# Optimization experiments

Measured on AMD Instinct MI355X. Metric: run time of the kernel, lower is better.

## Reference

```python
import jax, jax.numpy as jnp
import numpy as np

NUM_HEADS, KEY_DIM, BLOCK, HALO = 8, 64, 8, 4
KV_KERNEL = BLOCK + 2 * HALO  # 16
EMB = NUM_HEADS * KEY_DIM     # 512


def setup_inputs() -> dict:
    key = jax.random.key(0)
    k = jax.random.split(key, 6)
    stddev = KEY_DIM ** -0.5
    return {
        "x": jax.random.normal(k[0], (8, 64, 64, 512), jnp.float32),
        "wq": jax.random.normal(k[1], (512, EMB), jnp.float32) * 0.02,
        "wkv": jax.random.normal(k[2], (512, 2 * EMB), jnp.float32) * 0.02,
        "wout": jax.random.normal(k[3], (EMB, EMB), jnp.float32) * 0.02,
        "pos_w": jax.random.normal(k[4], (KEY_DIM, 2 * KV_KERNEL - 1), jnp.float32) * stddev,
        "pos_h": jax.random.normal(k[5], (KEY_DIM, 2 * KV_KERNEL - 1), jnp.float32) * stddev,
    }


def rel_to_abs(rel):
    # rel: [B, N, hh, ww, 2*pos_dim-1] -> [B, N, hh, ww, pos_dim]
    b, n, hh, ww, dim = rel.shape
    pos_dim = (dim + 1) // 2
    gap = pos_dim - ww
    flat = rel.reshape(b, n, hh, ww * dim)[:, :, :, ww - 1:-1]
    return flat.reshape(b, n, hh, ww, 2 * (pos_dim - 1))[:, :, :, :, gap:pos_dim + gap]


def halo_forward(x, wq, wkv, wout, pos_w, pos_h):
    B, H, W, C = x.shape
    h, w = H // BLOCK, W // BLOCK
    K = KV_KERNEL
    scale = 1.0 / jnp.sqrt(jnp.asarray(KEY_DIM, x.dtype))

    # Query: [B, hd, h, w, block^2, key_dim]
    q = (x @ wq) * scale
    q = q.reshape(B, h, BLOCK, w, BLOCK, NUM_HEADS, KEY_DIM)
    attn_q = q.transpose(0, 5, 1, 3, 2, 4, 6).reshape(B, NUM_HEADS, h, w, BLOCK * BLOCK, KEY_DIM)

    # Overlapping halo KV windows (im2col-style gather, like tf.image.extract_patches)
    kv = x @ wkv
    kv_p = jnp.pad(kv, ((0, 0), (HALO, HALO), (HALO, HALO), (0, 0)))
    idx_h = jnp.arange(h)[:, None] * BLOCK + jnp.arange(K)[None, :]  # [h, K]
    idx_w = jnp.arange(w)[:, None] * BLOCK + jnp.arange(K)[None, :]  # [w, K]
    patches = kv_p[:, idx_h][:, :, :, idx_w]          # [B, h, K, w, K, 2*EMB]
    patches = patches.transpose(0, 1, 3, 2, 4, 5)     # [B, h, w, K, K, 2*EMB]
    patches = patches.reshape(B, h, w, K * K, NUM_HEADS, 2 * KEY_DIM)
    patches = patches.transpose(0, 4, 1, 2, 3, 5)     # [B, hd, h, w, K^2, 2*key_dim]
    key_t, val = patches[..., :KEY_DIM], patches[..., KEY_DIM:]

    scores = jnp.einsum('bnhwqc,bnhwkc->bnhwqk', attn_q, key_t)  # [B,hd,h,w,bq,bk]

    # Relative position logits (width + height), query already carries qk_scale
    pos_q = attn_q.reshape(B, NUM_HEADS * h * w, BLOCK, BLOCK, KEY_DIM)
    rel_w = rel_to_abs(pos_q @ pos_w)                                      # [B,N,hb,wb,K]
    rel_h = rel_to_abs(pos_q.transpose(0, 1, 3, 2, 4) @ pos_h)
    rel_h = rel_h.transpose(0, 1, 3, 2, 4)                                 # [B,N,hb,wb,K]
    pos = rel_w[..., None, :] + rel_h[..., :, None]                        # [B,N,hb,wb,Kh,Kw]
    pos = pos.reshape(B, NUM_HEADS, h, w, BLOCK * BLOCK, K * K)

    attn = jax.nn.softmax(scores + pos, axis=-1)
    out = jnp.einsum('bnhwqk,bnhwkc->bnhwqc', attn, val)
    out = out.reshape(B, NUM_HEADS, h, w, BLOCK, BLOCK, KEY_DIM)
    out = out.transpose(0, 2, 4, 3, 5, 1, 6).reshape(B, H, W, EMB)
    return out @ wout


def reference(x, wq, wkv, wout, pos_w, pos_h):
    return halo_forward(x, wq, wkv, wout, pos_w, pos_h)
```

## Files before the change

kernel.cpp:

```cpp
#include <hip/hip_runtime.h>
#include <hip/hip_fp16.h>
#include <math.h>

typedef _Float16 f16x8 __attribute__((ext_vector_type(8)));
typedef _Float16 f16x4 __attribute__((ext_vector_type(4)));
typedef float    f32x4 __attribute__((ext_vector_type(4)));

#define M_TOT 32768
#define VROW  4608

__device__ __forceinline__ void gload16(const void* g, void* l) {
    __builtin_amdgcn_global_load_lds(
        (const __attribute__((address_space(1))) unsigned int*)g,
        (__attribute__((address_space(3))) unsigned int*)l, 16, 0, 0);
}

__device__ __forceinline__ f32x4 mfma32(f16x8 a, f16x8 b, f32x4 c) {
    return __builtin_amdgcn_mfma_f32_16x16x32_f16(a, b, c, 0, 0, 0);
}

__global__ __launch_bounds__(256) void conv_x(const float* __restrict__ x,
                                              __half* __restrict__ y) {
    const size_t i = ((size_t)blockIdx.x * 256 + threadIdx.x) * 8;
    float4 a = *(const float4*)&x[i];
    float4 b = *(const float4*)&x[i + 4];
    __half2 h[4];
    h[0] = __floats2half2_rn(a.x, a.y);
    h[1] = __floats2half2_rn(a.z, a.w);
    h[2] = __floats2half2_rn(b.x, b.y);
    h[3] = __floats2half2_rn(b.z, b.w);
    *(float4*)&y[i] = *(float4*)h;
}

__global__ __launch_bounds__(256) void conv_w(const float* __restrict__ wq,
                                              const float* __restrict__ wkv,
                                              const float* __restrict__ wout,
                                              __half* __restrict__ wT,
                                              __half* __restrict__ woT) {
    const int id = blockIdx.x * 256 + threadIdx.x;
    const int nr = id >> 9, k = id & 511;
    if (nr < 512) {
        wT[(size_t)nr * 512 + k]  = __float2half(wq[k * 512 + nr] * 0.125f);
    } else if (nr < 1536) {
        wT[(size_t)nr * 512 + k]  = __float2half(wkv[k * 1024 + (nr - 512)]);
    } else {
        woT[(size_t)(nr - 1536) * 512 + k] = __float2half(wout[k * 512 + (nr - 1536)]);
    }
}

__global__ __launch_bounds__(256) void pos_prep(const float* __restrict__ posw,
                                                const float* __restrict__ posh,
                                                __half* __restrict__ posT) {
    const int id = blockIdx.x * 256 + threadIdx.x;
    const int tb = id >> 11, idx = (id >> 6) & 31, d = id & 63;
    const float* src = tb ? posh : posw;
    posT[id] = __float2half((idx < 31) ? src[d * 31 + idx] : 0.f);
}

__global__ __launch_bounds__(256) void vborder(__half* __restrict__ vTp) {
    const int id = blockIdx.x * 256 + threadIdx.x;
    const int row = id >> 7, rem = id & 127;
    const int y = rem >> 1, side = rem & 1;
    f16x4 z = {(_Float16)0.f, (_Float16)0.f, (_Float16)0.f, (_Float16)0.f};
    *(f16x4*)(vTp + (size_t)row * VROW + y * 72 + side * 68) = z;
}

template <int MODE, int NBN>
__global__ __launch_bounds__(256) void mfma_gemm(
    const __half* __restrict__ A, const __half* __restrict__ Bt,
    __half* __restrict__ q16, __half* __restrict__ k16, __half* __restrict__ vTp,
    float* __restrict__ outf)
{
    __shared__ __align__(16) char As[128 * 128];
    __shared__ __align__(16) char Bs[128 * 128];

    const int t = threadIdx.x;
    const int l = t & 63, w = t >> 6;
    const int wr = w >> 1, wc = w & 1;
    const int lr = l & 15, hi = l >> 4;

    const int bid = blockIdx.x;
    const int xcd = bid & 7, loc = bid >> 3;
    const int bm  = xcd * 32 + (loc & 31);
    const int bn  = loc >> 5;

    f32x4 acc[4][4];
    #pragma unroll
    for (int i = 0; i < 4; ++i)
        #pragma unroll
        for (int j = 0; j < 4; ++j) acc[i][j] = (f32x4){0.f, 0.f, 0.f, 0.f};

    const int scid_row[4] = { (t * 16) >> 7, (256 * 16 + t * 16) >> 7,
                              (512 * 16 + t * 16) >> 7, (768 * 16 + t * 16) >> 7 };
    const int sch = (t & 7);

    for (int k0 = 0; k0 < 512; k0 += 64) {
        #pragma unroll
        for (int it = 0; it < 4; ++it) {
            const int row = it * 32 + (t >> 3);
            const int kk  = k0 + ((sch ^ (row & 7)) * 8);
            gload16(A + (size_t)(bm * 128 + row) * 512 + kk,
                    As + (it * 256 + w * 64) * 16);
        }
        #pragma unroll
        for (int it = 0; it < 4; ++it) {
            const int row = it * 32 + (t >> 3);
            const int kk  = k0 + ((sch ^ (row & 7)) * 8);
            gload16(Bt + (size_t)(bn * 128 + row) * 512 + kk,
                    Bs + (it * 256 + w * 64) * 16);
        }
        __syncthreads();

        #pragma unroll
        for (int dc = 0; dc < 2; ++dc) {
            f16x8 af[4], bf[4];
            #pragma unroll
            for (int i = 0; i < 4; ++i) {
                const int ra = wr * 64 + i * 16 + lr;
                af[i] = *(const f16x8*)(As + ra * 128 + (((dc * 4 + hi) ^ (ra & 7)) * 16));
            }
            #pragma unroll
            for (int j = 0; j < 4; ++j) {
                const int rb = wc * 64 + j * 16 + lr;
                bf[j] = *(const f16x8*)(Bs + rb * 128 + (((dc * 4 + hi) ^ (rb & 7)) * 16));
            }
            #pragma unroll
            for (int i = 0; i < 4; ++i)
                #pragma unroll
                for (int j = 0; j < 4; ++j)
                    acc[i][j] = mfma32(af[i], bf[j], acc[i][j]);
        }
        __syncthreads();
    }

    const int lq = hi;
    #pragma unroll
    for (int i = 0; i < 4; ++i) {
        #pragma unroll
        for (int j = 0; j < 4; ++j) {
            const int row0 = bm * 128 + wr * 64 + i * 16 + lq * 4;
            const int col  = bn * 128 + wc * 64 + j * 16 + lr;
            if (MODE == 1) {
                #pragma unroll
                for (int r = 0; r < 4; ++r)
                    outf[(size_t)(row0 + r) * 512 + col] = acc[i][j][r];
            } else if (bn < 4) {
                #pragma unroll
                for (int r = 0; r < 4; ++r)
                    q16[(size_t)(row0 + r) * 512 + col] = __float2half(acc[i][j][r]);
            } else if (wc == 0) {
                const int head = bn - 4, d2 = j * 16 + lr;
                #pragma unroll
                for (int r = 0; r < 4; ++r)
                    k16[(size_t)(row0 + r) * 512 + head * 64 + d2] = __float2half(acc[i][j][r]);
            } else {
                const int head = bn - 4, d2 = j * 16 + lr;
                const int bb = row0 >> 12, pix = row0 & 4095;
                const int py = pix >> 6, px = pix & 63;
                f16x4 pv;
                #pragma unroll
                for (int r = 0; r < 4; ++r) pv[r] = (_Float16)acc[i][j][r];
                *(f16x4*)(vTp + ((size_t)((bb * 8 + head) * 64 + d2)) * VROW + py * 72 + px + 4) = pv;
            }
        }
    }
}

__global__ __launch_bounds__(256, 3) void halo_attn(
    const __half* __restrict__ qbuf, const __half* __restrict__ kbuf,
    const __half* __restrict__ vTp, const __half* __restrict__ posT,
    const __half* __restrict__ zp, __half* __restrict__ obuf)
{
    __shared__ __align__(16) char KP[64 * 520];
    __shared__ float RWT[32][68];
    __shared__ float RHT[32][68];
    __shared__ float red[4][64];
    __shared__ float red2[4][64];

    const int hw = blockIdx.x;
    const int wg = (hw & 7) * 512 + (hw >> 3);
    const int wb = wg & 7, hb = (wg >> 3) & 7, n = (wg >> 6) & 7, b = wg >> 9;
    const int t = threadIdx.x;
    const int l = t & 63, g = t >> 6;
    const int hi = l >> 4, c15 = l & 15;

    #pragma unroll
    for (int it = 0; it < 8; ++it) {
        const int cid = it * 256 + t;
        const int S = cid * 16;
        const int row = S >> 7;
        const int d0h = (((S & 127) >> 4) ^ (row & 7)) * 8;
        const int ky = hb * 8 - 4 + (row >> 4);
        const int kx = wb * 8 - 4 + (row & 15);
        const bool ok = ((unsigned)ky < 64u) && ((unsigned)kx < 64u);
        const __half* src = ok ? (kbuf + ((size_t)((b * 64 + ky) * 64 + kx)) * 512 + n * 64 + d0h)
                               : zp;
        gload16(src, KP + (it * 256 + g * 64) * 16);
    }

    f16x8 vfrag[8];
    {
        const __half* vrow = vTp + ((size_t)((b * 8 + n) * 64 + g * 16 + c15)) * VROW;
        const int xoff = wb * 8 + (hi & 1) * 8;
        #pragma unroll
        for (int kc = 0; kc < 8; ++kc) {
            const int ki = kc * 2 + (hi >> 1);
            const int y = hb * 8 - 4 + ki;
            const __half* p = ((unsigned)y < 64u) ? (vrow + y * 72 + xoff) : zp;
            vfrag[kc] = *(const f16x8*)p;
        }
    }

    f16x8 qreg[4][2];
    #pragma unroll
    for (int qf = 0; qf < 4; ++qf) {
        const int q = qf * 16 + c15;
        const size_t pix = (size_t)((b * 64 + hb * 8 + (q >> 3)) * 64 + wb * 8 + (q & 7));
        #pragma unroll
        for (int dc = 0; dc < 2; ++dc)
            qreg[qf][dc] = *(const f16x8*)(qbuf + pix * 512 + n * 64 + dc * 32 + hi * 8);
    }

    {
        const int tb = g >> 1, ih = g & 1;
        f32x4 accp[4];
        #pragma unroll
        for (int qf = 0; qf < 4; ++qf) accp[qf] = (f32x4){0.f, 0.f, 0.f, 0.f};
        #pragma unroll
        for (int dc = 0; dc < 2; ++dc) {
            const f16x8 a = *(const f16x8*)(posT + tb * 2048 + (ih * 16 + c15) * 64 + dc * 32 + hi * 8);
            #pragma unroll
            for (int qf = 0; qf < 4; ++qf)
                accp[qf] = mfma32(a, qreg[qf][dc], accp[qf]);
        }
        float (*dst)[68] = tb ? RHT : RWT;
        #pragma unroll
        for (int qf = 0; qf < 4; ++qf)
            #pragma unroll
            for (int r = 0; r < 4; ++r)
                dst[ih * 16 + hi * 4 + r][qf * 16 + c15] = accp[qf][r];
    }
    __syncthreads();

    f32x4 accs[4][4];
    #pragma unroll
    for (int kf = 0; kf < 4; ++kf)
        #pragma unroll
        for (int qf = 0; qf < 4; ++qf) accs[kf][qf] = (f32x4){0.f, 0.f, 0.f, 0.f};

    __builtin_amdgcn_s_setprio(1);
    #pragma unroll
    for (int kf = 0; kf < 4; ++kf) {
        const int row = g * 64 + kf * 16 + c15;
        #pragma unroll
        for (int dc = 0; dc < 2; ++dc) {
            const int off = (row * 128 + dc * 64 + hi * 16) ^ ((row & 7) << 4);
            f16x8 a = *(const f16x8*)(KP + off);
            #pragma unroll
            for (int qf = 0; qf < 4; ++qf)
                accs[kf][qf] = mfma32(a, qreg[qf][dc], accs[kf][qf]);
        }
    }
    __builtin_amdgcn_s_setprio(0);

    float mq[4];
    #pragma unroll
    for (int qf = 0; qf < 4; ++qf) {
        const int q = qf * 16 + c15;
        const int qj = q & 7, qi = q >> 3;
        float pa[4], pb[4];
        #pragma unroll
        for (int r = 0; r < 4; ++r)  pa[r] = RWT[hi * 4 + r - qj + 15][q];
        #pragma unroll
        for (int kf = 0; kf < 4; ++kf) pb[kf] = RHT[g * 4 + kf - qi + 15][q];
        float mm = -1e30f;
        #pragma unroll
        for (int kf = 0; kf < 4; ++kf)
            #pragma unroll
            for (int r = 0; r < 4; ++r) {
                const float s = accs[kf][qf][r] + pa[r] + pb[kf];
                accs[kf][qf][r] = s;
                mm = fmaxf(mm, s);
            }
        mm = fmaxf(mm, __shfl_xor(mm, 16));
        mm = fmaxf(mm, __shfl_xor(mm, 32));
        mq[qf] = mm;
    }
    if (l < 16) {
        #pragma unroll
        for (int qf = 0; qf < 4; ++qf) red[g][qf * 16 + l] = mq[qf];
    }
    __syncthreads();

    float sums[4];
    #pragma unroll
    for (int qf = 0; qf < 4; ++qf) {
        const int q = qf * 16 + c15;
        const float mfull = fmaxf(fmaxf(red[0][q], red[1][q]), fmaxf(red[2][q], red[3][q]));
        float ss = 0.f;
        #pragma unroll
        for (int kf = 0; kf < 4; ++kf)
            #pragma unroll
            for (int r = 0; r < 4; ++r) {
                const float p = __expf(accs[kf][qf][r] - mfull);
                accs[kf][qf][r] = p;
                ss += p;
            }
        ss += __shfl_xor(ss, 16);
        ss += __shfl_xor(ss, 32);
        sums[qf] = ss;
        #pragma unroll
        for (int kf = 0; kf < 4; ++kf) {
            __half2 h01 = __floats2half2_rn(accs[kf][qf][0], accs[kf][qf][1]);
            __half2 h23 = __floats2half2_rn(accs[kf][qf][2], accs[kf][qf][3]);
            uint2 wv;
            wv.x = *(unsigned*)&h01;
            wv.y = *(unsigned*)&h23;
            *(uint2*)(KP + q * 520 + (g * 64 + kf * 16 + hi * 4) * 2) = wv;
        }
    }
    if (l < 16) {
        #pragma unroll
        for (int qf = 0; qf < 4; ++qf) red2[g][qf * 16 + l] = sums[qf];
    }
    __syncthreads();

    f32x4 acco[4];
    #pragma unroll
    for (int qf = 0; qf < 4; ++qf) acco[qf] = (f32x4){0.f, 0.f, 0.f, 0.f};
    __builtin_amdgcn_s_setprio(1);
    #pragma unroll
    for (int kc = 0; kc < 8; ++kc) {
        const f16x8 bf = vfrag[kc];
        #pragma unroll
        for (int qf = 0; qf < 4; ++qf) {
            const char* pp = KP + (qf * 16 + c15) * 520 + kc * 64 + hi * 16;
            const f16x4 p0 = *(const f16x4*)pp;
            const f16x4 p1 = *(const f16x4*)(pp + 8);
            const f16x8 af = __builtin_shufflevector(p0, p1, 0, 1, 2, 3, 4, 5, 6, 7);
            acco[qf] = mfma32(af, bf, acco[qf]);
        }
    }
    __builtin_amdgcn_s_setprio(0);

    #pragma unroll
    for (int qf = 0; qf < 4; ++qf) {
        #pragma unroll
        for (int r = 0; r < 4; ++r) {
            const int q = qf * 16 + hi * 4 + r;
            const float den = red2[0][q] + red2[1][q] + red2[2][q] + red2[3][q];
            const float v = acco[qf][r] / den;
            const size_t pix = (size_t)((b * 64 + hb * 8 + (q >> 3)) * 64 + wb * 8 + (q & 7));
            obuf[pix * 512 + n * 64 + g * 16 + c15] = __float2half(v);
        }
    }
}

extern "C" void kernel_launch(void* const* d_in, const int* in_sizes, int n_in,
                              void* d_out, int out_size, void* d_ws, size_t ws_size,
                              hipStream_t stream)
{
    const float* x    = (const float*)d_in[0];
    const float* wq   = (const float*)d_in[1];
    const float* wkv  = (const float*)d_in[2];
    const float* wout = (const float*)d_in[3];
    const float* posw = (const float*)d_in[4];
    const float* posh = (const float*)d_in[5];
    float* out = (float*)d_out;

    const size_t NPIX = (size_t)M_TOT * 512;
    const size_t NVTP = (size_t)64 * 64 * VROW;
    __half* x16  = (__half*)d_ws;
    __half* wT   = x16 + NPIX;
    __half* woT  = wT + (size_t)1536 * 512;
    __half* q16  = woT + (size_t)512 * 512;
    __half* k16  = q16 + NPIX;
    __half* vTp  = k16 + NPIX;
    __half* o16  = vTp + NVTP;
    __half* zp   = o16 + NPIX;
    __half* posT = zp + 128;

    hipMemsetAsync(zp, 0, 256, stream);

    conv_x<<<(M_TOT * 512) / (256 * 8), 256, 0, stream>>>(x, x16);
    conv_w<<<(2048 * 512) / 256, 256, 0, stream>>>(wq, wkv, wout, wT, woT);
    pos_prep<<<16, 256, 0, stream>>>(posw, posh, posT);
    vborder<<<2048, 256, 0, stream>>>(vTp);

    mfma_gemm<0, 12><<<3072, 256, 0, stream>>>(x16, wT, q16, k16, vTp, nullptr);

    halo_attn<<<4096, 256, 0, stream>>>(q16, k16, vTp, posT, zp, o16);

    mfma_gemm<1, 4><<<1024, 256, 0, stream>>>(o16, woT, nullptr, nullptr, nullptr, out);
}
```

Baseline: 211.4 us.

## Fuse prep kernels, shrink attention LDS to fp16 pos tables, use exp2

```diff
diff --git a/kernel.cpp b/kernel.cpp
--- a/kernel.cpp
+++ b/kernel.cpp
@@ -8,6 +8,7 @@
 
 #define M_TOT 32768
 #define VROW  4608
+#define LOG2E 1.44269504088896f
 
 __device__ __forceinline__ void gload16(const void* g, void* l) {
     __builtin_amdgcn_global_load_lds(
@@ -19,50 +20,51 @@
     return __builtin_amdgcn_mfma_f32_16x16x32_f16(a, b, c, 0, 0, 0);
 }
 
-__global__ __launch_bounds__(256) void conv_x(const float* __restrict__ x,
-                                              __half* __restrict__ y) {
-    const size_t i = ((size_t)blockIdx.x * 256 + threadIdx.x) * 8;
-    float4 a = *(const float4*)&x[i];
-    float4 b = *(const float4*)&x[i + 4];
-    __half2 h[4];
-    h[0] = __floats2half2_rn(a.x, a.y);
-    h[1] = __floats2half2_rn(a.z, a.w);
-    h[2] = __floats2half2_rn(b.x, b.y);
-    h[3] = __floats2half2_rn(b.z, b.w);
-    *(float4*)&y[i] = *(float4*)h;
-}
-
-__global__ __launch_bounds__(256) void conv_w(const float* __restrict__ wq,
-                                              const float* __restrict__ wkv,
-                                              const float* __restrict__ wout,
-                                              __half* __restrict__ wT,
-                                              __half* __restrict__ woT) {
-    const int id = blockIdx.x * 256 + threadIdx.x;
-    const int nr = id >> 9, k = id & 511;
-    if (nr < 512) {
-        wT[(size_t)nr * 512 + k]  = __float2half(wq[k * 512 + nr] * 0.125f);
-    } else if (nr < 1536) {
-        wT[(size_t)nr * 512 + k]  = __float2half(wkv[k * 1024 + (nr - 512)]);
+__global__ __launch_bounds__(256) void prep(
+    const float* __restrict__ x, const float* __restrict__ wq,
+    const float* __restrict__ wkv, const float* __restrict__ wout,
+    const float* __restrict__ posw, const float* __restrict__ posh,
+    __half* __restrict__ x16, __half* __restrict__ wT, __half* __restrict__ woT,
+    __half* __restrict__ posT, __half* __restrict__ vTp, __half* __restrict__ zp)
+{
+    const int bid = blockIdx.x, t = threadIdx.x;
+    if (bid < 8192) {
+        const size_t i = ((size_t)bid * 256 + t) * 8;
+        float4 a = *(const float4*)&x[i];
+        float4 b = *(const float4*)&x[i + 4];
+        __half2 h[4];
+        h[0] = __floats2half2_rn(a.x, a.y);
+        h[1] = __floats2half2_rn(a.z, a.w);
+        h[2] = __floats2half2_rn(b.x, b.y);
+        h[3] = __floats2half2_rn(b.z, b.w);
+        *(float4*)&x16[i] = *(float4*)h;
+    } else if (bid < 12288) {
+        const int id = (bid - 8192) * 256 + t;
+        const int nr = id >> 9, k = id & 511;
+        if (nr < 512) {
+            wT[(size_t)nr * 512 + k] = __float2half(wq[k * 512 + nr] * (0.125f * LOG2E));
+        } else if (nr < 1536) {
+            wT[(size_t)nr * 512 + k] = __float2half(wkv[k * 1024 + (nr - 512)]);
+        } else {
+            woT[(size_t)(nr - 1536) * 512 + k] = __float2half(wout[k * 512 + (nr - 1536)]);
+        }
+    } else if (bid < 14336) {
+        const int id = (bid - 12288) * 256 + t;
+        const int row = id >> 7, rem = id & 127;
+        const int y = rem >> 1, side = rem & 1;
+        f16x4 z = {(_Float16)0.f, (_Float16)0.f, (_Float16)0.f, (_Float16)0.f};
+        *(f16x4*)(vTp + (size_t)row * VROW + y * 72 + side * 68) = z;
+    } else if (bid < 14352) {
+        const int id = (bid - 14336) * 256 + t;
+        const int tb = id >> 11, idx = (id >> 6) & 31, d = id & 63;
+        const float* src = tb ? posh : posw;
+        posT[id] = __float2half((idx < 31) ? src[d * 31 + idx] : 0.f);
     } else {
-        woT[(size_t)(nr - 1536) * 512 + k] = __float2half(wout[k * 512 + (nr - 1536)]);
-    }
-}
-
-__global__ __launch_bounds__(256) void pos_prep(const float* __restrict__ posw,
-                                                const float* __restrict__ posh,
-                                                __half* __restrict__ posT) {
-    const int id = blockIdx.x * 256 + threadIdx.x;
-    const int tb = id >> 11, idx = (id >> 6) & 31, d = id & 63;
-    const float* src = tb ? posh : posw;
-    posT[id] = __float2half((idx < 31) ? src[d * 31 + idx] : 0.f);
-}
-
-__global__ __launch_bounds__(256) void vborder(__half* __restrict__ vTp) {
-    const int id = blockIdx.x * 256 + threadIdx.x;
-    const int row = id >> 7, rem = id & 127;
-    const int y = rem >> 1, side = rem & 1;
-    f16x4 z = {(_Float16)0.f, (_Float16)0.f, (_Float16)0.f, (_Float16)0.f};
-    *(f16x4*)(vTp + (size_t)row * VROW + y * 72 + side * 68) = z;
+        if (t < 16) {
+            float4 z = make_float4(0.f, 0.f, 0.f, 0.f);
+            *(float4*)(zp + t * 8) = z;
+        }
+    }
 }
 
 template <int MODE, int NBN>
@@ -90,8 +92,6 @@
         #pragma unroll
         for (int j = 0; j < 4; ++j) acc[i][j] = (f32x4){0.f, 0.f, 0.f, 0.f};
 
-    const int scid_row[4] = { (t * 16) >> 7, (256 * 16 + t * 16) >> 7,
-                              (512 * 16 + t * 16) >> 7, (768 * 16 + t * 16) >> 7 };
     const int sch = (t & 7);
 
     for (int k0 = 0; k0 < 512; k0 += 64) {
@@ -166,16 +166,18 @@
     }
 }
 
-__global__ __launch_bounds__(256, 3) void halo_attn(
+__global__ __launch_bounds__(256, 4) void halo_attn(
     const __half* __restrict__ qbuf, const __half* __restrict__ kbuf,
     const __half* __restrict__ vTp, const __half* __restrict__ posT,
     const __half* __restrict__ zp, __half* __restrict__ obuf)
 {
     __shared__ __align__(16) char KP[64 * 520];
-    __shared__ float RWT[32][68];
-    __shared__ float RHT[32][68];
+    __shared__ __align__(16) char POSB[6336];
     __shared__ float red[4][64];
-    __shared__ float red2[4][64];
+
+    __half* RW = (__half*)POSB;
+    __half* RH = (__half*)(POSB + 3168);
+    float (*red2)[64] = (float(*)[64])POSB;
 
     const int hw = blockIdx.x;
     const int wg = (hw & 7) * 512 + (hw >> 3);
@@ -233,12 +235,15 @@
             for (int qf = 0; qf < 4; ++qf)
                 accp[qf] = mfma32(a, qreg[qf][dc], accp[qf]);
         }
-        float (*dst)[68] = tb ? RHT : RWT;
+        __half* dst = tb ? RH : RW;
         #pragma unroll
         for (int qf = 0; qf < 4; ++qf)
             #pragma unroll
-            for (int r = 0; r < 4; ++r)
-                dst[ih * 16 + hi * 4 + r][qf * 16 + c15] = accp[qf][r];
+            for (int r = 0; r < 4; ++r) {
+                const unsigned idx8 = (unsigned)(ih * 16 + hi * 4 + r) - 8u;
+                if (idx8 < 23u)
+                    dst[idx8 * 66 + qf * 16 + c15] = __float2half(accp[qf][r]);
+            }
     }
     __syncthreads();
 
@@ -270,9 +275,9 @@
         const int qj = q & 7, qi = q >> 3;
         float pa[4], pb[4];
         #pragma unroll
-        for (int r = 0; r < 4; ++r)  pa[r] = RWT[hi * 4 + r - qj + 15][q];
-        #pragma unroll
-        for (int kf = 0; kf < 4; ++kf) pb[kf] = RHT[g * 4 + kf - qi + 15][q];
+        for (int r = 0; r < 4; ++r)  pa[r] = __half2float(RW[(hi * 4 + r + 7 - qj) * 66 + q]);
+        #pragma unroll
+        for (int kf = 0; kf < 4; ++kf) pb[kf] = __half2float(RH[(g * 4 + kf + 7 - qi) * 66 + q]);
         float mm = -1e30f;
         #pragma unroll
         for (int kf = 0; kf < 4; ++kf)
@@ -302,7 +307,7 @@
         for (int kf = 0; kf < 4; ++kf)
             #pragma unroll
             for (int r = 0; r < 4; ++r) {
-                const float p = __expf(accs[kf][qf][r] - mfull);
+                const float p = exp2f(accs[kf][qf][r] - mfull);
                 accs[kf][qf][r] = p;
                 ss += p;
             }
@@ -349,7 +354,7 @@
         for (int r = 0; r < 4; ++r) {
             const int q = qf * 16 + hi * 4 + r;
             const float den = red2[0][q] + red2[1][q] + red2[2][q] + red2[3][q];
-            const float v = acco[qf][r] / den;
+            const float v = acco[qf][r] * __builtin_amdgcn_rcpf(den);
             const size_t pix = (size_t)((b * 64 + hb * 8 + (q >> 3)) * 64 + wb * 8 + (q & 7));
             obuf[pix * 512 + n * 64 + g * 16 + c15] = __float2half(v);
         }
@@ -380,12 +385,8 @@
     __half* zp   = o16 + NPIX;
     __half* posT = zp + 128;
 
-    hipMemsetAsync(zp, 0, 256, stream);
-
-    conv_x<<<(M_TOT * 512) / (256 * 8), 256, 0, stream>>>(x, x16);
-    conv_w<<<(2048 * 512) / 256, 256, 0, stream>>>(wq, wkv, wout, wT, woT);
-    pos_prep<<<16, 256, 0, stream>>>(posw, posh, posT);
-    vborder<<<2048, 256, 0, stream>>>(vTp);
+    prep<<<14353, 256, 0, stream>>>(x, wq, wkv, wout, posw, posh,
+                                    x16, wT, woT, posT, vTp, zp);
 
     mfma_gemm<0, 12><<<3072, 256, 0, stream>>>(x16, wT, q16, k16, vTp, nullptr);
 
```

New measurement: 215.0 us (median of 2 runs). About the same (+1.7%).
